# Performance work log

Hardware: AMD Instinct MI355X
Metric: run time of the kernel (lower is better)

Reference implementation:

```python
import jax, jax.numpy as jnp
import numpy as np

B, Tu, Tm, Tz = 32, 128, 128, 32
V, H, E = 10000, 512, 128
S = E + H  # state_size


def setup_inputs() -> dict:
    key = jax.random.key(0)
    ks = jax.random.split(key, 24)
    u_input = jax.random.randint(ks[0], (B, Tu), 0, V)
    m_input = jax.random.randint(ks[1], (B, Tm), 0, V)
    pv_z_idx = jax.random.randint(ks[2], (B, Tz), 0, V)
    inp = {
        'u_input': u_input,
        'u_input_1hot': jax.nn.one_hot(u_input, V, dtype=jnp.float32),
        'u_hiddens': jax.random.normal(ks[3], (B, Tu, H), jnp.float32),
        'm_input': m_input,
        'm_input_1hot': jax.nn.one_hot(m_input, V, dtype=jnp.float32),
        'm_hiddens': jax.random.normal(ks[4], (B, Tm, H), jnp.float32),
        'pv_z_prob': jax.nn.softmax(jax.random.normal(ks[5], (B, Tz, V), jnp.float32), axis=-1),
        'pv_z_hidden': jax.random.normal(ks[6], (B, Tz, H), jnp.float32),
        'pv_z_idx': pv_z_idx,
        'emb_zt': jax.random.normal(ks[7], (B, 1, E), jnp.float32),
        'last_hidden': jax.random.normal(ks[8], (1, B, H), jnp.float32),
        # Attn params (concat attention: v . tanh(W [h; enc]))
        'W_attn': jax.random.normal(ks[9], (H, 2 * H), jnp.float32) * 0.02,
        'b_attn': jnp.zeros((H,), jnp.float32),
        'v_attn': jax.random.normal(ks[10], (H,), jnp.float32) * 0.05,
        # GRU params (torch gate order r,z,n)
        'W_ih': jax.random.normal(ks[11], (3 * H, S), jnp.float32) * 0.02,
        'W_hh': jax.random.normal(ks[12], (3 * H, H), jnp.float32) * 0.02,
        'b_ih': jnp.zeros((3 * H,), jnp.float32),
        'b_hh': jnp.zeros((3 * H,), jnp.float32),
        # generation / copy-score projections
        'W_gen': jax.random.normal(ks[13], (V, S), jnp.float32) * 0.02,
        'b_gen': jnp.zeros((V,), jnp.float32),
        'W_cpu': jax.random.normal(ks[14], (S, H), jnp.float32) * 0.02,
        'b_cpu': jnp.zeros((S,), jnp.float32),
        'W_cpm': jax.random.normal(ks[15], (S, H), jnp.float32) * 0.02,
        'b_cpm': jnp.zeros((S,), jnp.float32),
        'W_cppz': jax.random.normal(ks[16], (S, H), jnp.float32) * 0.02,
        'b_cppz': jnp.zeros((S,), jnp.float32),
    }
    return inp


def reference(u_input, u_input_1hot, u_hiddens, m_input, m_input_1hot, m_hiddens,
              pv_z_prob, pv_z_hidden, pv_z_idx, emb_zt, last_hidden,
              W_attn, b_attn, v_attn, W_ih, W_hh, b_ih, b_hh,
              W_gen, b_gen, W_cpu, b_cpu, W_cpm, b_cpm, W_cppz, b_cppz):
    Bv, Tuv, Vv = u_input_1hot.shape
    Tmv = m_hiddens.shape[1]
    t_input = emb_zt  # [B,1,E] (enable_selc_read=False)

    # ---- concat attention over [u; m; pv_z] hiddens ----
    enc = jnp.concatenate([u_hiddens, m_hiddens, pv_z_hidden], axis=1)  # [B,T,H]
    h0 = jnp.transpose(last_hidden, (1, 0, 2))  # [B,1,H]
    hid_rep = jnp.broadcast_to(h0, (Bv, enc.shape[1], h0.shape[2]))
    energy = jnp.tanh(jnp.einsum('bth,gh->btg', jnp.concatenate([hid_rep, enc], axis=2), W_attn) + b_attn)
    attn_w = jax.nn.softmax(jnp.einsum('bth,h->bt', energy, v_attn), axis=1)
    context = jnp.einsum('bt,bth->bh', attn_w, enc)[:, None, :]  # [B,1,H]

    # ---- single GRU step (torch gate order r,z,n) ----
    x = jnp.concatenate([t_input, context], axis=2)[:, 0, :]  # [B,E+H]
    h = h0[:, 0, :]
    gi = x @ W_ih.T + b_ih
    gh = h @ W_hh.T + b_hh
    i_r, i_z, i_n = jnp.split(gi, 3, axis=1)
    h_r, h_z, h_n = jnp.split(gh, 3, axis=1)
    r = jax.nn.sigmoid(i_r + h_r)
    z = jax.nn.sigmoid(i_z + h_z)
    n = jnp.tanh(i_n + r * h_n)
    h_new = (1.0 - z) * n + z * h  # [B,H]
    gru_out = h_new[:, None, :]
    last_hidden_new = h_new[None, :, :]

    # ---- generation + copy scores ----
    st = jnp.concatenate([h_new, t_input[:, 0, :]], axis=1)  # [B,E+H]
    score_g = st @ W_gen.T + b_gen  # [B,V]
    sc_u = jnp.einsum('bts,bs->bt', jnp.tanh(jnp.einsum('bth,sh->bts', u_hiddens, W_cpu) + b_cpu), st)
    sc_m = jnp.einsum('bts,bs->bt', jnp.tanh(jnp.einsum('bth,sh->bts', m_hiddens, W_cpm) + b_cpm), st)
    sc_pz = jnp.einsum('bts,bs->bt', jnp.tanh(jnp.einsum('bth,sh->bts', pv_z_hidden, W_cppz) + b_cppz), st)
    probs = jax.nn.softmax(jnp.concatenate([score_g, sc_u, sc_m, sc_pz], axis=1), axis=1)

    p_g = probs[:, :Vv]
    p_u = probs[:, Vv:Vv + Tuv]
    p_m = probs[:, Vv + Tuv:Vv + Tuv + Tmv]
    p_pz = probs[:, Vv + Tuv + Tmv:]
    prob_out = (p_g
                + jnp.einsum('bt,btv->bv', p_u, u_input_1hot)
                + jnp.einsum('bt,btv->bv', p_m, m_input_1hot)
                + jnp.einsum('bt,btv->bv', p_pz, pv_z_prob))
    return (prob_out, last_hidden_new, gru_out)
```

## Files before the change

kernel.cpp:

```cpp
#include <hip/hip_runtime.h>
#include <math.h>

#define B   32
#define TU  128
#define TM  128
#define TZ  32
#define TENC 288
#define V   10000
#define H   512
#define E   128
#define S   640
#define G3  1536
#define NLOG (V + TENC)

#define WS_Q      0
#define WS_SCORE  (WS_Q + B*H)
#define WS_CTX    (WS_SCORE + B*TENC)
#define WS_GI     (WS_CTX + B*H)
#define WS_GH     (WS_GI + B*G3)
#define WS_ST     (WS_GH + B*G3)
#define WS_LOGIT  (WS_ST + B*S)
#define WS_PCOPY  (WS_LOGIT + B*NLOG)
#define WS_F_TOTAL (WS_PCOPY + B*TENC)

#define BF_WA2  0
#define BF_WCP  (BF_WA2 + 512*512)
#define BF_ENC  (BF_WCP + 3*640*512)
#define BF_ST   (BF_ENC + B*TENC*H)
#define BF_TANH (BF_ST + B*S)

typedef __attribute__((ext_vector_type(8))) short bf16x8_t;
typedef __attribute__((ext_vector_type(4))) float f32x4_t;
typedef __attribute__((ext_vector_type(16))) float f32x16_t;

__device__ __forceinline__ float fast_tanh(float x) {
    return 1.f - 2.f / (__expf(2.f * x) + 1.f);
}

__device__ __forceinline__ unsigned short f2bf(float x) {
    unsigned int u = __float_as_uint(x);
    u += 0x7fffu + ((u >> 16) & 1u);
    return (unsigned short)(u >> 16);
}

__device__ __forceinline__ float bf2f(unsigned short u) {
    return __uint_as_float(((unsigned int)u) << 16);
}

__device__ __forceinline__ bf16x8_t cvt8(const float* p) {
    float4 a = *(const float4*)(p);
    float4 b = *(const float4*)(p + 4);
    bf16x8_t r;
    r[0] = (short)f2bf(a.x); r[1] = (short)f2bf(a.y);
    r[2] = (short)f2bf(a.z); r[3] = (short)f2bf(a.w);
    r[4] = (short)f2bf(b.x); r[5] = (short)f2bf(b.y);
    r[6] = (short)f2bf(b.z); r[7] = (short)f2bf(b.w);
    return r;
}

__device__ __forceinline__ const float* enc_row(const float* u, const float* m,
                                                const float* pz, int b, int t) {
    if (t < TU) return u + ((size_t)b * TU + t) * H;
    if (t < TU + TM) return m + ((size_t)b * TM + (t - TU)) * H;
    return pz + ((size_t)b * TZ + (t - TU - TM)) * H;
}

#define CVT_WA2_END  65536
#define CVT_TOTAL    (CVT_WA2_END + 3*81920)
#define CVTE_TOTAL   (B * TENC * 128)
#define CVT_ALL      (CVT_TOTAL + CVTE_TOTAL)
#define NMV          112
__global__ __launch_bounds__(256) void k_prep(const float* __restrict__ W_attn,
                                              const float* __restrict__ W_cpu,
                                              const float* __restrict__ W_cpm,
                                              const float* __restrict__ W_cppz,
                                              const float* __restrict__ u_h,
                                              const float* __restrict__ m_h,
                                              const float* __restrict__ pz_h,
                                              const float* __restrict__ last_h,
                                              const float* __restrict__ emb,
                                              const float* __restrict__ W_hh,
                                              const float* __restrict__ W_ih,
                                              const float* __restrict__ b_attn,
                                              const float* __restrict__ b_hh,
                                              const float* __restrict__ b_ih,
                                              float* __restrict__ ws,
                                              unsigned short* __restrict__ bf) {
    int blk = blockIdx.x, tid = threadIdx.x;
    __shared__ float redmv[4][64][16];
    if (blk < NMV) {
        int wave = tid >> 6, lane = tid & 63;
        int m = lane & 31, khalf = lane >> 5;
        f32x16_t acc = {};
        int n;
        if (blk < 16) {
            n = blk * 32 + m;
            const float* aptr = last_h + (size_t)m * H + khalf * 8;
            const float* bptr = W_attn + (size_t)n * 1024 + khalf * 8;
            for (int k0 = wave * 128; k0 < wave * 128 + 128; k0 += 16)
                acc = __builtin_amdgcn_mfma_f32_32x32x16_bf16(cvt8(aptr + k0),
                                                              cvt8(bptr + k0), acc, 0, 0, 0);
        } else if (blk < 64) {
            n = (blk - 16) * 32 + m;
            const float* aptr = last_h + (size_t)m * H + khalf * 8;
            const float* bptr = W_hh + (size_t)n * H + khalf * 8;
            for (int k0 = wave * 128; k0 < wave * 128 + 128; k0 += 16)
                acc = __builtin_amdgcn_mfma_f32_32x32x16_bf16(cvt8(aptr + k0),
                                                              cvt8(bptr + k0), acc, 0, 0, 0);
        } else {
            n = (blk - 64) * 32 + m;
            const float* aptr = emb + (size_t)m * E + khalf * 8;
            const float* bptr = W_ih + (size_t)n * S + khalf * 8;
            for (int k0 = wave * 32; k0 < wave * 32 + 32; k0 += 16)
                acc = __builtin_amdgcn_mfma_f32_32x32x16_bf16(cvt8(aptr + k0),
                                                              cvt8(bptr + k0), acc, 0, 0, 0);
        }
#pragma unroll
        for (int r = 0; r < 16; ++r) redmv[wave][lane][r] = acc[r];
        __syncthreads();
        if (wave == 0) {
#pragma unroll
            for (int r = 0; r < 16; ++r) {
                float v = redmv[0][lane][r] + redmv[1][lane][r] +
                          redmv[2][lane][r] + redmv[3][lane][r];
                int row = (r & 3) + 8 * (r >> 2) + 4 * khalf;
                if (blk < 16)      ws[WS_Q  + row * H  + n] = v + b_attn[n];
                else if (blk < 64) ws[WS_GH + row * G3 + n] = v + b_hh[n];
                else               ws[WS_GI + row * G3 + n] = v + b_ih[n];
            }
        }
        return;
    }
    int idx = (blk - NMV) * 256 + tid;
    if (idx >= CVT_ALL) return;
    const float* src;
    unsigned short* dst;
    if (idx < CVT_WA2_END) {
        int g = idx >> 7, c4 = idx & 127;
        int k = c4 * 4, kt = k >> 5, kin = k & 31;
        src = W_attn + (size_t)g * 1024 + 512 + k;
        dst = bf + BF_WA2 + kt * (512 * 32) + g * 32 + kin;
    } else if (idx < CVT_TOTAL) {
        int r = idx - CVT_WA2_END;
        int seg = r / 81920, q = r % 81920;
        int s = q >> 7, c4 = q & 127;
        int k = c4 * 4, kt = k >> 5, kin = k & 31;
        const float* s0 = (seg == 0) ? W_cpu : (seg == 1) ? W_cpm : W_cppz;
        src = s0 + (size_t)s * 512 + k;
        dst = bf + BF_WCP + seg * 327680 + kt * (640 * 32) + s * 32 + kin;
    } else {
        int e = idx - CVT_TOTAL;
        int b = e / (TENC * 128);
        int r = e % (TENC * 128);
        int t = r >> 7, c4 = r & 127;
        int k = c4 * 4, kt = k >> 5, kin = k & 31;
        src = enc_row(u_h, m_h, pz_h, b, t) + k;
        dst = bf + BF_ENC + (((size_t)b * 16 + kt) * TENC + t) * 32 + kin;
    }
    float4 v = *(const float4*)src;
    ushort4 o;
    o.x = f2bf(v.x); o.y = f2bf(v.y); o.z = f2bf(v.z); o.w = f2bf(v.w);
    *(ushort4*)dst = o;
}

__global__ __launch_bounds__(256) void k_enc_mfma(const unsigned short* __restrict__ bf,
                                                  const float* __restrict__ v_attn,
                                                  const float* __restrict__ b_cpu,
                                                  const float* __restrict__ b_cpm,
                                                  const float* __restrict__ b_cppz,
                                                  float* __restrict__ ws,
                                                  unsigned short* __restrict__ bft) {
    __shared__ __attribute__((aligned(16))) unsigned short lds_w[640 * 32];
    __shared__ __attribute__((aligned(16))) unsigned short lds_a[32 * 32];
    __shared__ float red[4][32];
    int blk = blockIdx.x;
    int typeC = (blk >= 288);
    int idx = typeC ? blk - 288 : blk;
    int b = idx / 9, t0 = (idx % 9) * 32;
    int tid = threadIdx.x, wave = tid >> 6, lane = tid & 63;
    int n16 = lane & 15, quad = lane >> 4;
    const unsigned short* asrc0 =
        bf + BF_ENC + (((size_t)b * 16) * TENC + t0) * 32;
    if (!typeC) {
        f32x4_t acc[2][8];
#pragma unroll
        for (int tl = 0; tl < 2; ++tl)
#pragma unroll
            for (int j = 0; j < 8; ++j) acc[tl][j] = (f32x4_t){0.f, 0.f, 0.f, 0.f};
        for (int kt = 0; kt < 16; ++kt) {
            const unsigned short* wsrc = bf + BF_WA2 + (size_t)kt * (512 * 32);
#pragma unroll
            for (int c = 0; c < 8; ++c) {
                int u = (c * 256 + tid) * 8;
                *(bf16x8_t*)&lds_w[u] = *(const bf16x8_t*)&wsrc[u];
            }
            if (tid < 128) {
                int u = tid * 8;
                *(bf16x8_t*)&lds_a[u] =
                    *(const bf16x8_t*)&asrc0[(size_t)kt * TENC * 32 + u];
            }
            __syncthreads();
            bf16x8_t a0 = *(const bf16x8_t*)&lds_a[n16 * 32 + quad * 8];
            bf16x8_t a1 = *(const bf16x8_t*)&lds_a[(n16 + 16) * 32 + quad * 8];
#pragma unroll
            for (int j = 0; j < 8; ++j) {
                bf16x8_t bb = *(const bf16x8_t*)
                    &lds_w[((wave * 8 + j) * 16 + n16) * 32 + quad * 8];
                acc[0][j] = __builtin_amdgcn_mfma_f32_16x16x32_bf16(a0, bb, acc[0][j], 0, 0, 0);
                acc[1][j] = __builtin_amdgcn_mfma_f32_16x16x32_bf16(a1, bb, acc[1][j], 0, 0, 0);
            }
            __syncthreads();
        }
        float sval[2][4] = {{0.f, 0.f, 0.f, 0.f}, {0.f, 0.f, 0.f, 0.f}};
#pragma unroll
        for (int j = 0; j < 8; ++j) {
            int g = (wave * 8 + j) * 16 + n16;
            float q = ws[WS_Q + b * H + g];
            float va = v_attn[g];
#pragma unroll
            for (int tl = 0; tl < 2; ++tl)
#pragma unroll
                for (int r = 0; r < 4; ++r)
                    sval[tl][r] += fast_tanh(acc[tl][j][r] + q) * va;
        }
#pragma unroll
        for (int tl = 0; tl < 2; ++tl)
#pragma unroll
            for (int r = 0; r < 4; ++r)
#pragma unroll
                for (int off = 8; off > 0; off >>= 1)
                    sval[tl][r] += __shfl_down(sval[tl][r], off, 64);
        if (n16 == 0)
#pragma unroll
            for (int tl = 0; tl < 2; ++tl)
#pragma unroll
                for (int r = 0; r < 4; ++r)
                    red[wave][tl * 16 + quad * 4 + r] = sval[tl][r];
        __syncthreads();
        if (tid < 32)
            ws[WS_SCORE + b * TENC + t0 + tid] =
                red[0][tid] + red[1][tid] + red[2][tid] + red[3][tid];
    } else {
        int seg = (t0 < TU) ? 0 : (t0 < TU + TM) ? 1 : 2;
        const float* bias = (seg == 0) ? b_cpu : (seg == 1) ? b_cpm : b_cppz;
        f32x4_t acc[2][10];
#pragma unroll
        for (int tl = 0; tl < 2; ++tl)
#pragma unroll
            for (int j = 0; j < 10; ++j) acc[tl][j] = (f32x4_t){0.f, 0.f, 0.f, 0.f};
        for (int kt = 0; kt < 16; ++kt) {
            const unsigned short* wsrc =
                bf + BF_WCP + seg * 327680 + (size_t)kt * (640 * 32);
#pragma unroll
            for (int c = 0; c < 10; ++c) {
                int u = (c * 256 + tid) * 8;
                *(bf16x8_t*)&lds_w[u] = *(const bf16x8_t*)&wsrc[u];
            }
            if (tid < 128) {
                int u = tid * 8;
                *(bf16x8_t*)&lds_a[u] =
                    *(const bf16x8_t*)&asrc0[(size_t)kt * TENC * 32 + u];
            }
            __syncthreads();
            bf16x8_t a0 = *(const bf16x8_t*)&lds_a[n16 * 32 + quad * 8];
            bf16x8_t a1 = *(const bf16x8_t*)&lds_a[(n16 + 16) * 32 + quad * 8];
#pragma unroll
            for (int j = 0; j < 10; ++j) {
                bf16x8_t bb = *(const bf16x8_t*)
                    &lds_w[((wave * 10 + j) * 16 + n16) * 32 + quad * 8];
                acc[0][j] = __builtin_amdgcn_mfma_f32_16x16x32_bf16(a0, bb, acc[0][j], 0, 0, 0);
                acc[1][j] = __builtin_amdgcn_mfma_f32_16x16x32_bf16(a1, bb, acc[1][j], 0, 0, 0);
            }
            __syncthreads();
        }
#pragma unroll
        for (int j = 0; j < 10; ++j) {
            int s = (wave * 10 + j) * 16 + n16;
            float bi = bias[s];
#pragma unroll
            for (int tl = 0; tl < 2; ++tl)
#pragma unroll
                for (int r = 0; r < 4; ++r) {
                    int t = t0 + tl * 16 + quad * 4 + r;
                    bft[BF_TANH + ((size_t)b * TENC + t) * S + s] =
                        f2bf(fast_tanh(acc[tl][j][r] + bi));
                }
        }
    }
}

__global__ __launch_bounds__(256) void k_softmax_ctx(const unsigned short* __restrict__ bf,
                                                     float* __restrict__ ws) {
    int b = blockIdx.x, tid = threadIdx.x;
    __shared__ float wsm[TENC];
    __shared__ float red1[4], red2[4];
    float local = -1e30f;
    for (int t = tid; t < TENC; t += 256) {
        float s = ws[WS_SCORE + b * TENC + t];
        wsm[t] = s;
        local = fmaxf(local, s);
    }
    int lane = tid & 63, wv = tid >> 6;
    for (int off = 32; off > 0; off >>= 1) local = fmaxf(local, __shfl_down(local, off, 64));
    if (lane == 0) red1[wv] = local;
    __syncthreads();
    float mx = fmaxf(fmaxf(red1[0], red1[1]), fmaxf(red1[2], red1[3]));
    float ls = 0.f;
    for (int t = tid; t < TENC; t += 256) {
        float e = __expf(wsm[t] - mx);
        wsm[t] = e;
        ls += e;
    }
    for (int off = 32; off > 0; off >>= 1) ls += __shfl_down(ls, off, 64);
    if (lane == 0) red2[wv] = ls;
    __syncthreads();
    float inv = 1.f / (red2[0] + red2[1] + red2[2] + red2[3]);

    int h2 = tid * 2;
    int kt = h2 >> 5, hin = h2 & 31;
    const unsigned short* ep = bf + BF_ENC + ((size_t)b * 16 + kt) * TENC * 32 + hin;
    float a00 = 0.f, a01 = 0.f, a10 = 0.f, a11 = 0.f;
#pragma unroll 2
    for (int t = 0; t < TENC; t += 2) {
        ushort2 v0 = *(const ushort2*)(ep + (size_t)t * 32);
        ushort2 v1 = *(const ushort2*)(ep + (size_t)(t + 1) * 32);
        float w0 = wsm[t], w1 = wsm[t + 1];
        a00 += w0 * bf2f(v0.x); a10 += w0 * bf2f(v0.y);
        a01 += w1 * bf2f(v1.x); a11 += w1 * bf2f(v1.y);
    }
    ws[WS_CTX + b * H + h2]     = (a00 + a01) * inv;
    ws[WS_CTX + b * H + h2 + 1] = (a10 + a11) * inv;
}

__global__ __launch_bounds__(256) void k_gru_ctx(const float* __restrict__ W_ih,
                                                 float* __restrict__ ws) {
    int blk = blockIdx.x, tid = threadIdx.x;
    __shared__ float redmv[4][64][16];
    int wave = tid >> 6, lane = tid & 63;
    int m = lane & 31, khalf = lane >> 5;
    int n = blk * 32 + m;
    const float* aptr = ws + WS_CTX + (size_t)m * H + khalf * 8;
    const float* bptr = W_ih + (size_t)n * S + E + khalf * 8;
    f32x16_t acc = {};
    for (int k0 = wave * 128; k0 < wave * 128 + 128; k0 += 16)
        acc = __builtin_amdgcn_mfma_f32_32x32x16_bf16(cvt8(aptr + k0),
                                                      cvt8(bptr + k0), acc, 0, 0, 0);
#pragma unroll
    for (int r = 0; r < 16; ++r) redmv[wave][lane][r] = acc[r];
    __syncthreads();
    if (wave == 0) {
#pragma unroll
        for (int r = 0; r < 16; ++r) {
            float v = redmv[0][lane][r] + redmv[1][lane][r] +
                      redmv[2][lane][r] + redmv[3][lane][r];
            int row = (r & 3) + 8 * (r >> 2) + 4 * khalf;
            ws[WS_GI + row * G3 + n] += v;
        }
    }
}

__global__ __launch_bounds__(256) void k_combine(const float* __restrict__ emb,
                                                 const float* __restrict__ last_hidden,
                                                 float* __restrict__ ws,
                                                 unsigned short* __restrict__ bf,
                                                 float* __restrict__ out) {
    int i = blockIdx.x * 256 + threadIdx.x;
    int b = i >> 9, h = i & 511;
    float gi_r = ws[WS_GI + b * G3 + h];
    float gi_z = ws[WS_GI + b * G3 + H + h];
    float gi_n = ws[WS_GI + b * G3 + 2 * H + h];
    float gh_r = ws[WS_GH + b * G3 + h];
    float gh_z = ws[WS_GH + b * G3 + H + h];
    float gh_n = ws[WS_GH + b * G3 + 2 * H + h];
    float rr = 1.f / (1.f + __expf(-(gi_r + gh_r)));
    float zz = 1.f / (1.f + __expf(-(gi_z + gh_z)));
    float nn = fast_tanh(gi_n + rr * gh_n);
    float hp = last_hidden[b * H + h];
    float hn = (1.f - zz) * nn + zz * hp;
    out[V * B + b * H + h] = hn;
    out[V * B + B * H + b * H + h] = hn;
    ws[WS_ST + b * S + h] = hn;
    bf[BF_ST + b * S + h] = f2bf(hn);
    if (h < E) {
        float ev = emb[b * E + h];
        ws[WS_ST + b * S + H + h] = ev;
        bf[BF_ST + b * S + H + h] = f2bf(ev);
    }
}

__global__ __launch_bounds__(256) void k_logits(const unsigned short* __restrict__ bf,
                                                const float* __restrict__ W_gen,
                                                const float* __restrict__ b_gen,
                                                float* __restrict__ ws) {
    int blk = blockIdx.x, tid = threadIdx.x;
    __shared__ float shmem[4 * 64 * 16];
    int wave = tid >> 6, lane = tid & 63;
    if (blk < 576) {
        int b = blk / 18, t0 = (blk % 18) * 16;
        float* st_s = shmem;
        for (int i = tid; i < S; i += 256) st_s[i] = ws[WS_ST + b * S + i];
        __syncthreads();
#pragma unroll
        for (int tl = 0; tl < 4; ++tl) {
            int t = t0 + wave * 4 + tl;
            const unsigned short* row = bf + BF_TANH + ((size_t)b * TENC + t) * S;
            float acc = 0.f;
#pragma unroll
            for (int i = 0; i < 10; ++i) {
                int s = lane + 64 * i;
                acc += bf2f(row[s]) * st_s[s];
            }
            for (int off = 32; off > 0; off >>= 1) acc += __shfl_down(acc, off, 64);
            if (lane == 0) ws[WS_LOGIT + (size_t)b * NLOG + V + t] = acc;
        }
    } else {
        float (*redmv)[64][16] = (float (*)[64][16])shmem;
        int m = lane & 31, khalf = lane >> 5;
        int n = (blk - 576) * 32 + m;
        int nr = (n < V) ? n : (V - 1);
        const unsigned short* aptr = bf + BF_ST + (size_t)m * S + khalf * 8;
        const float* bptr = W_gen + (size_t)nr * S + khalf * 8;
        f32x16_t acc = {};
        for (int k0 = wave * 160; k0 < wave * 160 + 160; k0 += 16)
            acc = __builtin_amdgcn_mfma_f32_32x32x16_bf16(*(const bf16x8_t*)(aptr + k0),
                                                          cvt8(bptr + k0), acc, 0, 0, 0);
#pragma unroll
        for (int r = 0; r < 16; ++r) redmv[wave][lane][r] = acc[r];
        __syncthreads();
        if (wave == 0 && n < V) {
            float bg = b_gen[n];
#pragma unroll
            for (int r = 0; r < 16; ++r) {
                float v = redmv[0][lane][r] + redmv[1][lane][r] +
                          redmv[2][lane][r] + redmv[3][lane][r];
                int row = (r & 3) + 8 * (r >> 2) + 4 * khalf;
                ws[WS_LOGIT + (size_t)row * NLOG + n] = v + bg;
            }
        }
    }
}

__global__ __launch_bounds__(512) void k_softmax_scatter(const int* __restrict__ u_in,
                                                         const int* __restrict__ m_in,
                                                         float* __restrict__ ws,
                                                         float* __restrict__ out) {
    int b = blockIdx.x, tid = threadIdx.x;
    __shared__ float red1[8], red2[8];
    __shared__ float ex[NLOG];
    const float* lg = ws + WS_LOGIT + (size_t)b * NLOG;
    float mx = -1e30f;
    for (int i = tid; i < NLOG; i += 512) {
        float v = lg[i];
        ex[i] = v;
        mx = fmaxf(mx, v);
    }
    int lane = tid & 63, wv = tid >> 6;
    for (int off = 32; off > 0; off >>= 1) mx = fmaxf(mx, __shfl_down(mx, off, 64));
    if (lane == 0) red1[wv] = mx;
    __syncthreads();
    mx = red1[0];
#pragma unroll
    for (int w = 1; w < 8; ++w) mx = fmaxf(mx, red1[w]);
    float sm = 0.f;
    for (int i = tid; i < NLOG; i += 512) {
        float e = __expf(ex[i] - mx);
        ex[i] = e;
        sm += e;
    }
    for (int off = 32; off > 0; off >>= 1) sm += __shfl_down(sm, off, 64);
    if (lane == 0) red2[wv] = sm;
    __syncthreads();
    sm = red2[0];
#pragma unroll
    for (int w = 1; w < 8; ++w) sm += red2[w];
    float inv = 1.f / sm;
    for (int i = tid; i < V; i += 512) out[b * V + i] = ex[i] * inv;
    __syncthreads();
    if (tid < TU + TM) {
        int idx = (tid < TU) ? u_in[b * TU + tid] : m_in[b * TM + (tid - TU)];
        atomicAdd(&out[(size_t)b * V + idx], ex[V + tid] * inv);
    } else if (tid < TENC) {
        ws[WS_PCOPY + b * TENC + tid] = ex[V + tid] * inv;
    }
}

__global__ __launch_bounds__(256) void k_pv(const float* __restrict__ pvp,
                                            const float* __restrict__ ws,
                                            float* __restrict__ out) {
    int b = blockIdx.y;
    int v = blockIdx.x * 256 + threadIdx.x;
    __shared__ float p[TZ];
    if (threadIdx.x < TZ) p[threadIdx.x] = ws[WS_PCOPY + b * TENC + TU + TM + threadIdx.x];
    __syncthreads();
    if (v >= V) return;
    float acc = 0.f;
#pragma unroll 4
    for (int t = 0; t < TZ; ++t) acc += p[t] * pvp[((size_t)b * TZ + t) * V + v];
    out[(size_t)b * V + v] += acc;
}

extern "C" void kernel_launch(void* const* d_in, const int* in_sizes, int n_in,
                              void* d_out, int out_size, void* d_ws, size_t ws_size,
                              hipStream_t stream) {
    const int*   u_input   = (const int*)d_in[0];
    const float* u_h       = (const float*)d_in[2];
    const int*   m_input   = (const int*)d_in[3];
    const float* m_h       = (const float*)d_in[5];
    const float* pv_prob   = (const float*)d_in[6];
    const float* pz_h      = (const float*)d_in[7];
    const float* emb       = (const float*)d_in[9];
    const float* last_h    = (const float*)d_in[10];
    const float* W_attn    = (const float*)d_in[11];
    const float* b_attn    = (const float*)d_in[12];
    const float* v_attn    = (const float*)d_in[13];
    const float* W_ih      = (const float*)d_in[14];
    const float* W_hh      = (const float*)d_in[15];
    const float* b_ih      = (const float*)d_in[16];
    const float* b_hh      = (const float*)d_in[17];
    const float* W_gen     = (const float*)d_in[18];
    const float* b_gen     = (const float*)d_in[19];
    const float* W_cpu     = (const float*)d_in[20];
    const float* b_cpu     = (const float*)d_in[21];
    const float* W_cpm     = (const float*)d_in[22];
    const float* b_cpm     = (const float*)d_in[23];
    const float* W_cppz    = (const float*)d_in[24];
    const float* b_cppz    = (const float*)d_in[25];
    float* ws  = (float*)d_ws;
    unsigned short* bf = (unsigned short*)(ws + WS_F_TOTAL);
    float* out = (float*)d_out;

    hipLaunchKernelGGL(k_prep, dim3(NMV + CVT_ALL / 256), dim3(256), 0, stream,
                       W_attn, W_cpu, W_cpm, W_cppz, u_h, m_h, pz_h,
                       last_h, emb, W_hh, W_ih, b_attn, b_hh, b_ih, ws, bf);
    hipLaunchKernelGGL(k_enc_mfma, dim3(576), dim3(256), 0, stream,
                       bf, v_attn, b_cpu, b_cpm, b_cppz, ws, bf);
    hipLaunchKernelGGL(k_softmax_ctx, dim3(B), dim3(256), 0, stream, bf, ws);
    hipLaunchKernelGGL(k_gru_ctx, dim3(48), dim3(256), 0, stream, W_ih, ws);
    hipLaunchKernelGGL(k_combine, dim3(64), dim3(256), 0, stream, emb, last_h, ws, bf, out);
    hipLaunchKernelGGL(k_logits, dim3(576 + 313), dim3(256), 0, stream, bf, W_gen, b_gen, ws);
    hipLaunchKernelGGL(k_softmax_scatter, dim3(B), dim3(512), 0, stream,
                       u_input, m_input, ws, out);
    hipLaunchKernelGGL(k_pv, dim3(40, B), dim3(256), 0, stream, pv_prob, ws, out);
}
```

Measured before the change: 468.1 us.

## Double-buffer enc MFMA loads with 512 threads, fuse GRU context and combine kernels

The encoder MFMA kernel now runs 512 threads per block and prefetches the next k-tile of weights and activations into registers while the current tile is computed, then writes it to LDS. This hides global load latency behind the MFMA work. The GRU context matmul and the gate combine are merged into one 16-block kernel that computes all three gates per hidden slice and applies the nonlinearity directly, removing one launch and a workspace round trip. The embedding copy into the state buffer moves into the prep kernel, and the pv loop unroll goes from 4 to 8; the fused GRU kernel has fewer blocks and so less parallelism.

Measured after the change: 465.4 us. No clear change (-0.6%).

```diff
diff --git a/kernel.cpp b/kernel.cpp
--- a/kernel.cpp
+++ b/kernel.cpp
@@ -69,6 +69,7 @@
 #define CVT_TOTAL    (CVT_WA2_END + 3*81920)
 #define CVTE_TOTAL   (B * TENC * 128)
 #define CVT_ALL      (CVT_TOTAL + CVTE_TOTAL)
+#define CVT_EMBST    (CVT_ALL + B*E/4)
 #define NMV          112
 __global__ __launch_bounds__(256) void k_prep(const float* __restrict__ W_attn,
                                               const float* __restrict__ W_cpu,
@@ -132,7 +133,17 @@
         return;
     }
     int idx = (blk - NMV) * 256 + tid;
-    if (idx >= CVT_ALL) return;
+    if (idx >= CVT_EMBST) return;
+    if (idx >= CVT_ALL) {
+        int e = idx - CVT_ALL;
+        int b = e >> 5, unit = e & 31;
+        float4 v = *(const float4*)(emb + b * E + unit * 4);
+        *(float4*)&ws[WS_ST + b * S + H + unit * 4] = v;
+        ushort4 o;
+        o.x = f2bf(v.x); o.y = f2bf(v.y); o.z = f2bf(v.z); o.w = f2bf(v.w);
+        *(ushort4*)&bf[BF_ST + b * S + H + unit * 4] = o;
+        return;
+    }
     const float* src;
     unsigned short* dst;
     if (idx < CVT_WA2_END) {
@@ -163,7 +174,7 @@
     *(ushort4*)dst = o;
 }
 
-__global__ __launch_bounds__(256) void k_enc_mfma(const unsigned short* __restrict__ bf,
+__global__ __launch_bounds__(512) void k_enc_mfma(const unsigned short* __restrict__ bf,
                                                   const float* __restrict__ v_attn,
                                                   const float* __restrict__ b_cpu,
                                                   const float* __restrict__ b_cpm,
@@ -172,7 +183,7 @@
                                                   unsigned short* __restrict__ bft) {
     __shared__ __attribute__((aligned(16))) unsigned short lds_w[640 * 32];
     __shared__ __attribute__((aligned(16))) unsigned short lds_a[32 * 32];
-    __shared__ float red[4][32];
+    __shared__ float red[8][32];
     int blk = blockIdx.x;
     int typeC = (blk >= 288);
     int idx = typeC ? blk - 288 : blk;
@@ -182,39 +193,57 @@
     const unsigned short* asrc0 =
         bf + BF_ENC + (((size_t)b * 16) * TENC + t0) * 32;
     if (!typeC) {
-        f32x4_t acc[2][8];
+        bf16x8_t rw0, rw1, rw2, rw3, ra;
+        const unsigned short* wb = bf + BF_WA2;
+        rw0 = *(const bf16x8_t*)&wb[(0 * 512 + tid) * 8];
+        rw1 = *(const bf16x8_t*)&wb[(1 * 512 + tid) * 8];
+        rw2 = *(const bf16x8_t*)&wb[(2 * 512 + tid) * 8];
+        rw3 = *(const bf16x8_t*)&wb[(3 * 512 + tid) * 8];
+        if (tid < 128) ra = *(const bf16x8_t*)&asrc0[tid * 8];
+        *(bf16x8_t*)&lds_w[(0 * 512 + tid) * 8] = rw0;
+        *(bf16x8_t*)&lds_w[(1 * 512 + tid) * 8] = rw1;
+        *(bf16x8_t*)&lds_w[(2 * 512 + tid) * 8] = rw2;
+        *(bf16x8_t*)&lds_w[(3 * 512 + tid) * 8] = rw3;
+        if (tid < 128) *(bf16x8_t*)&lds_a[tid * 8] = ra;
+        __syncthreads();
+        f32x4_t acc[2][4];
 #pragma unroll
         for (int tl = 0; tl < 2; ++tl)
 #pragma unroll
-            for (int j = 0; j < 8; ++j) acc[tl][j] = (f32x4_t){0.f, 0.f, 0.f, 0.f};
+            for (int j = 0; j < 4; ++j) acc[tl][j] = (f32x4_t){0.f, 0.f, 0.f, 0.f};
         for (int kt = 0; kt < 16; ++kt) {
-            const unsigned short* wsrc = bf + BF_WA2 + (size_t)kt * (512 * 32);
-#pragma unroll
-            for (int c = 0; c < 8; ++c) {
-                int u = (c * 256 + tid) * 8;
-                *(bf16x8_t*)&lds_w[u] = *(const bf16x8_t*)&wsrc[u];
-            }
-            if (tid < 128) {
-                int u = tid * 8;
-                *(bf16x8_t*)&lds_a[u] =
-                    *(const bf16x8_t*)&asrc0[(size_t)kt * TENC * 32 + u];
-            }
-            __syncthreads();
+            if (kt < 15) {
+                const unsigned short* wsrc = wb + (size_t)(kt + 1) * (512 * 32);
+                rw0 = *(const bf16x8_t*)&wsrc[(0 * 512 + tid) * 8];
+                rw1 = *(const bf16x8_t*)&wsrc[(1 * 512 + tid) * 8];
+                rw2 = *(const bf16x8_t*)&wsrc[(2 * 512 + tid) * 8];
+                rw3 = *(const bf16x8_t*)&wsrc[(3 * 512 + tid) * 8];
+                if (tid < 128)
+                    ra = *(const bf16x8_t*)&asrc0[(size_t)(kt + 1) * TENC * 32 + tid * 8];
+            }
             bf16x8_t a0 = *(const bf16x8_t*)&lds_a[n16 * 32 + quad * 8];
             bf16x8_t a1 = *(const bf16x8_t*)&lds_a[(n16 + 16) * 32 + quad * 8];
 #pragma unroll
-            for (int j = 0; j < 8; ++j) {
+            for (int j = 0; j < 4; ++j) {
                 bf16x8_t bb = *(const bf16x8_t*)
-                    &lds_w[((wave * 8 + j) * 16 + n16) * 32 + quad * 8];
+                    &lds_w[((wave * 4 + j) * 16 + n16) * 32 + quad * 8];
                 acc[0][j] = __builtin_amdgcn_mfma_f32_16x16x32_bf16(a0, bb, acc[0][j], 0, 0, 0);
                 acc[1][j] = __builtin_amdgcn_mfma_f32_16x16x32_bf16(a1, bb, acc[1][j], 0, 0, 0);
             }
             __syncthreads();
+            if (kt < 15) {
+                *(bf16x8_t*)&lds_w[(0 * 512 + tid) * 8] = rw0;
+                *(bf16x8_t*)&lds_w[(1 * 512 + tid) * 8] = rw1;
+                *(bf16x8_t*)&lds_w[(2 * 512 + tid) * 8] = rw2;
+                *(bf16x8_t*)&lds_w[(3 * 512 + tid) * 8] = rw3;
+                if (tid < 128) *(bf16x8_t*)&lds_a[tid * 8] = ra;
+            }
+            __syncthreads();
         }
         float sval[2][4] = {{0.f, 0.f, 0.f, 0.f}, {0.f, 0.f, 0.f, 0.f}};
 #pragma unroll
-        for (int j = 0; j < 8; ++j) {
-            int g = (wave * 8 + j) * 16 + n16;
+        for (int j = 0; j < 4; ++j) {
+            int g = (wave * 4 + j) * 16 + n16;
             float q = ws[WS_Q + b * H + g];
             float va = v_attn[g];
 #pragma unroll
@@ -237,45 +266,69 @@
                 for (int r = 0; r < 4; ++r)
                     red[wave][tl * 16 + quad * 4 + r] = sval[tl][r];
         __syncthreads();
-        if (tid < 32)
-            ws[WS_SCORE + b * TENC + t0 + tid] =
-                red[0][tid] + red[1][tid] + red[2][tid] + red[3][tid];
+        if (tid < 32) {
+            float v = 0.f;
+#pragma unroll
+            for (int w = 0; w < 8; ++w) v += red[w][tid];
+            ws[WS_SCORE + b * TENC + t0 + tid] = v;
+        }
     } else {
         int seg = (t0 < TU) ? 0 : (t0 < TU + TM) ? 1 : 2;
         const float* bias = (seg == 0) ? b_cpu : (seg == 1) ? b_cpm : b_cppz;
-        f32x4_t acc[2][10];
+        const unsigned short* wb = bf + BF_WCP + seg * 327680;
+        bf16x8_t rw0, rw1, rw2, rw3, rw4, ra;
+        rw0 = *(const bf16x8_t*)&wb[(0 * 512 + tid) * 8];
+        rw1 = *(const bf16x8_t*)&wb[(1 * 512 + tid) * 8];
+        rw2 = *(const bf16x8_t*)&wb[(2 * 512 + tid) * 8];
+        rw3 = *(const bf16x8_t*)&wb[(3 * 512 + tid) * 8];
+        rw4 = *(const bf16x8_t*)&wb[(4 * 512 + tid) * 8];
+        if (tid < 128) ra = *(const bf16x8_t*)&asrc0[tid * 8];
+        *(bf16x8_t*)&lds_w[(0 * 512 + tid) * 8] = rw0;
+        *(bf16x8_t*)&lds_w[(1 * 512 + tid) * 8] = rw1;
+        *(bf16x8_t*)&lds_w[(2 * 512 + tid) * 8] = rw2;
+        *(bf16x8_t*)&lds_w[(3 * 512 + tid) * 8] = rw3;
+        *(bf16x8_t*)&lds_w[(4 * 512 + tid) * 8] = rw4;
+        if (tid < 128) *(bf16x8_t*)&lds_a[tid * 8] = ra;
+        __syncthreads();
+        f32x4_t acc[2][5];
 #pragma unroll
         for (int tl = 0; tl < 2; ++tl)
 #pragma unroll
-            for (int j = 0; j < 10; ++j) acc[tl][j] = (f32x4_t){0.f, 0.f, 0.f, 0.f};
+            for (int j = 0; j < 5; ++j) acc[tl][j] = (f32x4_t){0.f, 0.f, 0.f, 0.f};
         for (int kt = 0; kt < 16; ++kt) {
-            const unsigned short* wsrc =
-                bf + BF_WCP + seg * 327680 + (size_t)kt * (640 * 32);
-#pragma unroll
-            for (int c = 0; c < 10; ++c) {
-                int u = (c * 256 + tid) * 8;
-                *(bf16x8_t*)&lds_w[u] = *(const bf16x8_t*)&wsrc[u];
-            }
-            if (tid < 128) {
-                int u = tid * 8;
-                *(bf16x8_t*)&lds_a[u] =
-                    *(const bf16x8_t*)&asrc0[(size_t)kt * TENC * 32 + u];
-            }
-            __syncthreads();
+            if (kt < 15) {
+                const unsigned short* wsrc = wb + (size_t)(kt + 1) * (640 * 32);
+                rw0 = *(const bf16x8_t*)&wsrc[(0 * 512 + tid) * 8];
+                rw1 = *(const bf16x8_t*)&wsrc[(1 * 512 + tid) * 8];
+                rw2 = *(const bf16x8_t*)&wsrc[(2 * 512 + tid) * 8];
+                rw3 = *(const bf16x8_t*)&wsrc[(3 * 512 + tid) * 8];
+                rw4 = *(const bf16x8_t*)&wsrc[(4 * 512 + tid) * 8];
+                if (tid < 128)
+                    ra = *(const bf16x8_t*)&asrc0[(size_t)(kt + 1) * TENC * 32 + tid * 8];
+            }
             bf16x8_t a0 = *(const bf16x8_t*)&lds_a[n16 * 32 + quad * 8];
             bf16x8_t a1 = *(const bf16x8_t*)&lds_a[(n16 + 16) * 32 + quad * 8];
 #pragma unroll
-            for (int j = 0; j < 10; ++j) {
+            for (int j = 0; j < 5; ++j) {
                 bf16x8_t bb = *(const bf16x8_t*)
-                    &lds_w[((wave * 10 + j) * 16 + n16) * 32 + quad * 8];
+                    &lds_w[((wave * 5 + j) * 16 + n16) * 32 + quad * 8];
                 acc[0][j] = __builtin_amdgcn_mfma_f32_16x16x32_bf16(a0, bb, acc[0][j], 0, 0, 0);
                 acc[1][j] = __builtin_amdgcn_mfma_f32_16x16x32_bf16(a1, bb, acc[1][j], 0, 0, 0);
             }
             __syncthreads();
-        }
-#pragma unroll
-        for (int j = 0; j < 10; ++j) {
-            int s = (wave * 10 + j) * 16 + n16;
+            if (kt < 15) {
+                *(bf16x8_t*)&lds_w[(0 * 512 + tid) * 8] = rw0;
+                *(bf16x8_t*)&lds_w[(1 * 512 + tid) * 8] = rw1;
+                *(bf16x8_t*)&lds_w[(2 * 512 + tid) * 8] = rw2;
+                *(bf16x8_t*)&lds_w[(3 * 512 + tid) * 8] = rw3;
+                *(bf16x8_t*)&lds_w[(4 * 512 + tid) * 8] = rw4;
+                if (tid < 128) *(bf16x8_t*)&lds_a[tid * 8] = ra;
+            }
+            __syncthreads();
+        }
+#pragma unroll
+        for (int j = 0; j < 5; ++j) {
+            int s = (wave * 5 + j) * 16 + n16;
             float bi = bias[s];
 #pragma unroll
             for (int tl = 0; tl < 2; ++tl)
@@ -332,59 +385,57 @@
     ws[WS_CTX + b * H + h2 + 1] = (a10 + a11) * inv;
 }
 
-__global__ __launch_bounds__(256) void k_gru_ctx(const float* __restrict__ W_ih,
-                                                 float* __restrict__ ws) {
+__global__ __launch_bounds__(256) void k_gru2(const float* __restrict__ W_ih,
+                                              const float* __restrict__ last_hidden,
+                                              float* __restrict__ ws,
+                                              unsigned short* __restrict__ bf,
+                                              float* __restrict__ out) {
     int blk = blockIdx.x, tid = threadIdx.x;
     __shared__ float redmv[4][64][16];
     int wave = tid >> 6, lane = tid & 63;
     int m = lane & 31, khalf = lane >> 5;
-    int n = blk * 32 + m;
+    int h0 = blk * 32;
+    float vg[3][16];
     const float* aptr = ws + WS_CTX + (size_t)m * H + khalf * 8;
-    const float* bptr = W_ih + (size_t)n * S + E + khalf * 8;
-    f32x16_t acc = {};
-    for (int k0 = wave * 128; k0 < wave * 128 + 128; k0 += 16)
-        acc = __builtin_amdgcn_mfma_f32_32x32x16_bf16(cvt8(aptr + k0),
-                                                      cvt8(bptr + k0), acc, 0, 0, 0);
-#pragma unroll
-    for (int r = 0; r < 16; ++r) redmv[wave][lane][r] = acc[r];
-    __syncthreads();
+#pragma unroll
+    for (int gate = 0; gate < 3; ++gate) {
+        const float* bptr = W_ih + (size_t)(gate * H + h0 + m) * S + E + khalf * 8;
+        f32x16_t acc = {};
+        for (int k0 = wave * 128; k0 < wave * 128 + 128; k0 += 16)
+            acc = __builtin_amdgcn_mfma_f32_32x32x16_bf16(cvt8(aptr + k0),
+                                                          cvt8(bptr + k0), acc, 0, 0, 0);
+#pragma unroll
+        for (int r = 0; r < 16; ++r) redmv[wave][lane][r] = acc[r];
+        __syncthreads();
+        if (wave == 0) {
+#pragma unroll
+            for (int r = 0; r < 16; ++r)
+                vg[gate][r] = redmv[0][lane][r] + redmv[1][lane][r] +
+                              redmv[2][lane][r] + redmv[3][lane][r];
+        }
+        __syncthreads();
+    }
     if (wave == 0) {
+        int h = h0 + m;
 #pragma unroll
         for (int r = 0; r < 16; ++r) {
-            float v = redmv[0][lane][r] + redmv[1][lane][r] +
-                      redmv[2][lane][r] + redmv[3][lane][r];
-            int row = (r & 3) + 8 * (r >> 2) + 4 * khalf;
-            ws[WS_GI + row * G3 + n] += v;
-        }
-    }
-}
-
-__global__ __launch_bounds__(256) void k_combine(const float* __restrict__ emb,
-                                                 const float* __restrict__ last_hidden,
-                                                 float* __restrict__ ws,
-                                                 unsigned short* __restrict__ bf,
-                                                 float* __restrict__ out) {
-    int i = blockIdx.x * 256 + threadIdx.x;
-    int b = i >> 9, h = i & 511;
-    float gi_r = ws[WS_GI + b * G3 + h];
-    float gi_z = ws[WS_GI + b * G3 + H + h];
-    float gi_n = ws[WS_GI + b * G3 + 2 * H + h];
-    float gh_r = ws[WS_GH + b * G3 + h];
-    float gh_z = ws[WS_GH + b * G3 + H + h];
-    float gh_n = ws[WS_GH + b * G3 + 2 * H + h];
-    float rr = 1.f / (1.f + __expf(-(gi_r + gh_r)));
-    float zz = 1.f / (1.f + __expf(-(gi_z + gh_z)));
-    float nn = fast_tanh(gi_n + rr * gh_n);
-    float hp = last_hidden[b * H + h];
-    float hn = (1.f - zz) * nn + zz * hp;
-    out[V * B + b * H + h] = hn;
-    out[V * B + B * H + b * H + h] = hn;
-    ws[WS_ST + b * S + h] = hn;
-    bf[BF_ST + b * S + h] = f2bf(hn);
-    if (h < E) {
-        float ev = emb[b * E + h];
-        ws[WS_ST + b * S + H + h] = ev;
-        bf[BF_ST + b * S + H + h] = f2bf(ev);
+            int b = (r & 3) + 8 * (r >> 2) + 4 * khalf;
+            float gi_r = vg[0][r] + ws[WS_GI + b * G3 + h];
+            float gi_z = vg[1][r] + ws[WS_GI + b * G3 + H + h];
+            float gi_n = vg[2][r] + ws[WS_GI + b * G3 + 2 * H + h];
+            float gh_r = ws[WS_GH + b * G3 + h];
+            float gh_z = ws[WS_GH + b * G3 + H + h];
+            float gh_n = ws[WS_GH + b * G3 + 2 * H + h];
+            float rr = 1.f / (1.f + __expf(-(gi_r + gh_r)));
+            float zz = 1.f / (1.f + __expf(-(gi_z + gh_z)));
+            float nn = fast_tanh(gi_n + rr * gh_n);
+            float hp = last_hidden[b * H + h];
+            float hn = (1.f - zz) * nn + zz * hp;
+            out[V * B + b * H + h] = hn;
+            out[V * B + B * H + b * H + h] = hn;
+            ws[WS_ST + b * S + h] = hn;
+            bf[BF_ST + b * S + h] = f2bf(hn);
+        }
     }
 }
 
@@ -494,7 +545,7 @@
     __syncthreads();
     if (v >= V) return;
     float acc = 0.f;
-#pragma unroll 4
+#pragma unroll 8
     for (int t = 0; t < TZ; ++t) acc += p[t] * pvp[((size_t)b * TZ + t) * V + v];
     out[(size_t)b * V + v] += acc;
 }
@@ -529,14 +580,13 @@
     unsigned short* bf = (unsigned short*)(ws + WS_F_TOTAL);
     float* out = (float*)d_out;
 
-    hipLaunchKernelGGL(k_prep, dim3(NMV + CVT_ALL / 256), dim3(256), 0, stream,
+    hipLaunchKernelGGL(k_prep, dim3(NMV + (CVT_EMBST + 255) / 256), dim3(256), 0, stream,
                        W_attn, W_cpu, W_cpm, W_cppz, u_h, m_h, pz_h,
                        last_h, emb, W_hh, W_ih, b_attn, b_hh, b_ih, ws, bf);
-    hipLaunchKernelGGL(k_enc_mfma, dim3(576), dim3(256), 0, stream,
+    hipLaunchKernelGGL(k_enc_mfma, dim3(576), dim3(512), 0, stream,
                        bf, v_attn, b_cpu, b_cpm, b_cppz, ws, bf);
     hipLaunchKernelGGL(k_softmax_ctx, dim3(B), dim3(256), 0, stream, bf, ws);
-    hipLaunchKernelGGL(k_gru_ctx, dim3(48), dim3(256), 0, stream, W_ih, ws);
-    hipLaunchKernelGGL(k_combine, dim3(64), dim3(256), 0, stream, emb, last_h, ws, bf, out);
+    hipLaunchKernelGGL(k_gru2, dim3(16), dim3(256), 0, stream, W_ih, last_h, ws, bf, out);
     hipLaunchKernelGGL(k_logits, dim3(576 + 313), dim3(256), 0, stream, bf, W_gen, b_gen, ws);
     hipLaunchKernelGGL(k_softmax_scatter, dim3(B), dim3(512), 0, stream,
                        u_input, m_input, ws, out);
```
